# Kernel optimization log

Measured on AMD Instinct MI355X. Metric: run time of the kernel, lower is better.

## Reference

```python
import jax, jax.numpy as jnp
import numpy as np

GRID = 192          # grid_size (scaled up from the module's toy 32)
H = 0.1             # cell_size
VISC = 0.01         # viscosity
DT = 0.01           # config.time_step, passed as forward's dt
GRAV = 9.81


def setup_inputs() -> dict:
    key = jax.random.key(0)
    velocity_field = jax.random.normal(key, (3, GRID, GRID, GRID), dtype=jnp.float32)
    return {"velocity_field": velocity_field}


def _nb_sum(f):
    # 6-neighbor sum on the interior of the last three axes
    return (f[..., 2:, 1:-1, 1:-1] + f[..., :-2, 1:-1, 1:-1]
            + f[..., 1:-1, 2:, 1:-1] + f[..., 1:-1, :-2, 1:-1]
            + f[..., 1:-1, 1:-1, 2:] + f[..., 1:-1, 1:-1, :-2])


def _fluid_step(vel):
    N = GRID
    dt = DT
    # --- add_gravity ---
    vel = vel.at[2].add(-GRAV * dt)
    # --- advect: semi-Lagrangian backtrace + trilinear interpolation ---
    coords = jnp.arange(N, dtype=vel.dtype)
    X, Y, Z = jnp.meshgrid(coords, coords, coords, indexing='ij')
    pos = jnp.stack([X, Y, Z]) - vel * (dt / H)        # [3,N,N,N] backtraced positions
    pos = jnp.clip(pos, 0.0, float(N - 2))
    i0 = jnp.floor(pos).astype(jnp.int32)              # base corner, i1 = i0+1 <= N-1
    w1 = pos - i0.astype(vel.dtype)
    w0 = 1.0 - w1
    ix, iy, iz = i0[0], i0[1], i0[2]
    wx0, wy0, wz0 = w0[0], w0[1], w0[2]
    wx1, wy1, wz1 = w1[0], w1[1], w1[2]

    def g(di, dj, dk):
        return vel[:, ix + di, iy + dj, iz + dk]        # gather -> [3,N,N,N]

    vel = (g(0, 0, 0) * wx0 * wy0 * wz0 + g(0, 0, 1) * wx0 * wy0 * wz1
           + g(0, 1, 0) * wx0 * wy1 * wz0 + g(0, 1, 1) * wx0 * wy1 * wz1
           + g(1, 0, 0) * wx1 * wy0 * wz0 + g(1, 0, 1) * wx1 * wy0 * wz1
           + g(1, 1, 0) * wx1 * wy1 * wz0 + g(1, 1, 1) * wx1 * wy1 * wz1)
    # --- diffuse: 5 Jacobi sweeps on the interior ---
    alpha = VISC * dt / (H * H)
    inv = 1.0 / (1.0 + 6.0 * alpha)
    for _ in range(5):
        interior = (vel[:, 1:-1, 1:-1, 1:-1] + alpha * _nb_sum(vel)) * inv
        vel = vel.at[:, 1:-1, 1:-1, 1:-1].set(interior)
    # --- project: central-difference divergence, 20 Jacobi pressure sweeps, gradient subtract ---
    div = jnp.zeros((N, N, N), vel.dtype)
    div_int = ((vel[0, 2:, 1:-1, 1:-1] - vel[0, :-2, 1:-1, 1:-1])
               + (vel[1, 1:-1, 2:, 1:-1] - vel[1, 1:-1, :-2, 1:-1])
               + (vel[2, 1:-1, 1:-1, 2:] - vel[2, 1:-1, 1:-1, :-2])) / (2.0 * H)
    div = div.at[1:-1, 1:-1, 1:-1].set(div_int)
    p = jnp.zeros_like(div)
    for _ in range(20):
        p = p.at[1:-1, 1:-1, 1:-1].set((div[1:-1, 1:-1, 1:-1] + _nb_sum(p)) / 6.0)
    inv2h = 1.0 / (2.0 * H)
    vel = vel.at[0, 1:-1, 1:-1, 1:-1].add(-(p[2:, 1:-1, 1:-1] - p[:-2, 1:-1, 1:-1]) * inv2h)
    vel = vel.at[1, 1:-1, 1:-1, 1:-1].add(-(p[1:-1, 2:, 1:-1] - p[1:-1, :-2, 1:-1]) * inv2h)
    vel = vel.at[2, 1:-1, 1:-1, 1:-1].add(-(p[1:-1, 1:-1, 2:] - p[1:-1, 1:-1, :-2]) * inv2h)
    return vel


def reference(velocity_field):
    return _fluid_step(velocity_field)
```

## Files before the change

kernel.cpp:

```cpp
#include <hip/hip_runtime.h>
#include <hip/hip_fp16.h>


constexpr int   N      = 192;
constexpr int   N2     = N * N;
constexpr int   N3     = N * N * N;
constexpr float GDT    = 9.81f * 0.01f;
constexpr float SCL    = 0.01f / 0.1f;
constexpr float ALPHA  = 0.01f * 0.01f / (0.1f * 0.1f);
constexpr float INVDIF = 1.0f / (1.0f + 6.0f * ALPHA);
constexpr float INV2H  = 1.0f / (2.0f * 0.1f);
constexpr float SIXTH  = 1.0f / 6.0f;

constexpr int NT4 = (N3 / 4) / 256;
constexpr int SLAB = NT4 / 8;

__device__ __forceinline__ int swz(int b) {
    return (b & 7) * SLAB + (b >> 3);
}

__device__ __forceinline__ void decomp(int id, int& i, int& j, int& k0) {
    i = id / N2;
    const int r = id - i * N2;
    j = r / N;
    k0 = r - j * N;
}

union H4u { ushort4 u; __half h[4]; };
__device__ __forceinline__ float4 ldh4(const __half* p) {
    H4u t; t.u = *(const ushort4*)p;
    return make_float4(__half2float(t.h[0]), __half2float(t.h[1]),
                       __half2float(t.h[2]), __half2float(t.h[3]));
}
__device__ __forceinline__ void sth4(__half* p, float x, float y, float z, float w) {
    H4u t;
    t.h[0] = __float2half(x); t.h[1] = __float2half(y);
    t.h[2] = __float2half(z); t.h[3] = __float2half(w);
    *(ushort4*)p = t.u;
}
__device__ __forceinline__ float ldh(const __half* p) { return __half2float(*p); }

__global__ __launch_bounds__(192) void k_advect(const float* __restrict__ vin,
                                                float* __restrict__ vout) {
    __shared__ float s[27 * 192];

    const int k   = threadIdx.x;
    const int lin = blockIdx.y * 192 + blockIdx.x;
    const int x   = lin & 7;
    const int q   = lin >> 3;
    const int il  = q % 24;
    const int j   = q / 24;
    const int i   = x * 24 + il;
    const int id  = (i * N + j) * N + k;

    {
        const int rsub = threadIdx.x / 48;
        const int col  = (threadIdx.x - rsub * 48) * 4;
#pragma unroll
        for (int p = 0; p < 7; ++p) {
            const int r = p * 4 + rsub;
            if (r < 27) {
                const int c   = r / 9;
                const int rem = r - c * 9;
                const int di  = rem / 3;
                const int dj  = rem - di * 3;
                const int gi  = min(max(i + di - 1, 0), N - 1);
                const int gj  = min(max(j + dj - 1, 0), N - 1);
                *(float4*)&s[r * 192 + col] =
                    *(const float4*)&vin[c * N3 + gi * N2 + gj * N + col];
            }
        }
    }
    __syncthreads();

    const float vx = s[4 * 192 + k];
    const float vy = s[13 * 192 + k];
    const float vz = s[22 * 192 + k] - GDT;

    float px = (float)i - vx * SCL;
    float py = (float)j - vy * SCL;
    float pz = (float)k - vz * SCL;
    const float hi = (float)(N - 2);
    px = fminf(fmaxf(px, 0.0f), hi);
    py = fminf(fmaxf(py, 0.0f), hi);
    pz = fminf(fmaxf(pz, 0.0f), hi);

    const int ix = (int)px;
    const int iy = (int)py;
    const int iz = (int)pz;

    float g[3][8];
    const bool in = (ix >= i - 1) & (ix <= i) & (iy >= j - 1) & (iy <= j);
    if (in) {
        const int li = ix - i + 1;
        const int lj = iy - j + 1;
#pragma unroll
        for (int c = 0; c < 3; ++c) {
            const int r00 = ((c * 3 + li) * 3 + lj) * 192 + iz;
            const int r01 = r00 + 192;
            const int r10 = r00 + 3 * 192;
            const int r11 = r10 + 192;
            g[c][0] = s[r00];     g[c][1] = s[r00 + 1];
            g[c][2] = s[r01];     g[c][3] = s[r01 + 1];
            g[c][4] = s[r10];     g[c][5] = s[r10 + 1];
            g[c][6] = s[r11];     g[c][7] = s[r11 + 1];
        }
    } else {
        const int base = (ix * N + iy) * N + iz;
#pragma unroll
        for (int c = 0; c < 3; ++c) {
            const float* f = vin + c * N3 + base;
            g[c][0] = f[0];      g[c][1] = f[1];
            g[c][2] = f[N];      g[c][3] = f[N + 1];
            g[c][4] = f[N2];     g[c][5] = f[N2 + 1];
            g[c][6] = f[N2 + N]; g[c][7] = f[N2 + N + 1];
        }
    }

    const float wx1 = px - (float)ix, wy1 = py - (float)iy, wz1 = pz - (float)iz;
    const float wx0 = 1.0f - wx1,     wy0 = 1.0f - wy1,     wz0 = 1.0f - wz1;
    const float w000 = wx0 * wy0 * wz0;
    const float w001 = wx0 * wy0 * wz1;
    const float w010 = wx0 * wy1 * wz0;
    const float w011 = wx0 * wy1 * wz1;
    const float w100 = wx1 * wy0 * wz0;
    const float w101 = wx1 * wy0 * wz1;
    const float w110 = wx1 * wy1 * wz0;
    const float w111 = wx1 * wy1 * wz1;

#pragma unroll
    for (int c = 0; c < 3; ++c) {
        float r = g[c][0] * w000 + g[c][1] * w001
                + g[c][2] * w010 + g[c][3] * w011
                + g[c][4] * w100 + g[c][5] * w101
                + g[c][6] * w110 + g[c][7] * w111;
        if (c == 2) r -= GDT;
        vout[c * N3 + id] = r;
    }
}

__global__ __launch_bounds__(256) void k_diffuse4(const float* __restrict__ vin,
                                                  float* __restrict__ vout) {
    const int gtid = swz(blockIdx.x) * 256 + threadIdx.x;
    const int id   = gtid << 2;
    int i, j, k0; decomp(id, i, j, k0);
    const int b = blockIdx.y * N3 + id;

    const float4 c = *(const float4*)(vin + b);
    float4 out = c;
    if (i != 0 && i != N - 1 && j != 0 && j != N - 1) {
        const float4 ip = *(const float4*)(vin + b + N2);
        const float4 im = *(const float4*)(vin + b - N2);
        const float4 jp = *(const float4*)(vin + b + N);
        const float4 jm = *(const float4*)(vin + b - N);
        const float  km = (k0 > 0)     ? vin[b - 1] : 0.0f;
        const float  kp = (k0 < N - 4) ? vin[b + 4] : 0.0f;
        out.x = (c.x + ALPHA * (im.x + ip.x + jm.x + jp.x + km  + c.y)) * INVDIF;
        out.y = (c.y + ALPHA * (im.y + ip.y + jm.y + jp.y + c.x + c.z)) * INVDIF;
        out.z = (c.z + ALPHA * (im.z + ip.z + jm.z + jp.z + c.y + c.w)) * INVDIF;
        out.w = (c.w + ALPHA * (im.w + ip.w + jm.w + jp.w + c.z + kp )) * INVDIF;
        if (k0 == 0)     out.x = c.x;
        if (k0 == N - 4) out.w = c.w;
    }
    *(float4*)(vout + b) = out;
}

__global__ __launch_bounds__(256) void k_div4(const float* __restrict__ v,
                                              __half* __restrict__ dv) {
    const int gtid = swz(blockIdx.x) * 256 + threadIdx.x;
    const int id   = gtid << 2;
    int i, j, k0; decomp(id, i, j, k0);

    float ox = 0.f, oy = 0.f, oz = 0.f, ow = 0.f;
    if (i != 0 && i != N - 1 && j != 0 && j != N - 1) {
        const float4 xp = *(const float4*)(v + id + N2);
        const float4 xm = *(const float4*)(v + id - N2);
        const float4 yp = *(const float4*)(v + N3 + id + N);
        const float4 ym = *(const float4*)(v + N3 + id - N);
        const float4 z  = *(const float4*)(v + 2 * N3 + id);
        const float  zm = (k0 > 0)     ? v[2 * N3 + id - 1] : 0.0f;
        const float  zp = (k0 < N - 4) ? v[2 * N3 + id + 4] : 0.0f;
        ox = ((xp.x - xm.x) + (yp.x - ym.x) + (z.y - zm )) * INV2H;
        oy = ((xp.y - xm.y) + (yp.y - ym.y) + (z.z - z.x)) * INV2H;
        oz = ((xp.z - xm.z) + (yp.z - ym.z) + (z.w - z.y)) * INV2H;
        ow = ((xp.w - xm.w) + (yp.w - ym.w) + (zp  - z.z)) * INV2H;
        if (k0 == 0)     ox = 0.f;
        if (k0 == N - 4) ow = 0.f;
    }
    sth4(dv + id, ox, oy, oz, ow);
}

__global__ __launch_bounds__(256) void k_p2_4(const __half* __restrict__ dv,
                                              __half* __restrict__ p) {
    const int gtid = swz(blockIdx.x) * 256 + threadIdx.x;
    const int id   = gtid << 2;
    int i, j, k0; decomp(id, i, j, k0);

    float ox = 0.f, oy = 0.f, oz = 0.f, ow = 0.f;
    if (i != 0 && i != N - 1 && j != 0 && j != N - 1) {
        const float4 c  = ldh4(dv + id);
        const float4 ip = ldh4(dv + id + N2);
        const float4 im = ldh4(dv + id - N2);
        const float4 jp = ldh4(dv + id + N);
        const float4 jm = ldh4(dv + id - N);
        const float  km = (k0 > 0)     ? ldh(dv + id - 1) : 0.0f;
        const float  kp = (k0 < N - 4) ? ldh(dv + id + 4) : 0.0f;
        ox = (c.x + (im.x + ip.x + jm.x + jp.x + km  + c.y) * SIXTH) * SIXTH;
        oy = (c.y + (im.y + ip.y + jm.y + jp.y + c.x + c.z) * SIXTH) * SIXTH;
        oz = (c.z + (im.z + ip.z + jm.z + jp.z + c.y + c.w) * SIXTH) * SIXTH;
        ow = (c.w + (im.w + ip.w + jm.w + jp.w + c.z + kp ) * SIXTH) * SIXTH;
        if (k0 == 0)     ox = 0.f;
        if (k0 == N - 4) ow = 0.f;
    }
    sth4(p + id, ox, oy, oz, ow);
}

__global__ __launch_bounds__(256) void k_jacobi4(const __half* __restrict__ pin,
                                                 const __half* __restrict__ dv,
                                                 __half* __restrict__ pout) {
    const int gtid = swz(blockIdx.x) * 256 + threadIdx.x;
    const int id   = gtid << 2;
    int i, j, k0; decomp(id, i, j, k0);

    float ox = 0.f, oy = 0.f, oz = 0.f, ow = 0.f;
    if (i != 0 && i != N - 1 && j != 0 && j != N - 1) {
        const float4 c  = ldh4(pin + id);
        const float4 ip = ldh4(pin + id + N2);
        const float4 im = ldh4(pin + id - N2);
        const float4 jp = ldh4(pin + id + N);
        const float4 jm = ldh4(pin + id - N);
        const float4 d  = ldh4(dv + id);
        const float  km = (k0 > 0)     ? ldh(pin + id - 1) : 0.0f;
        const float  kp = (k0 < N - 4) ? ldh(pin + id + 4) : 0.0f;
        ox = (d.x + im.x + ip.x + jm.x + jp.x + km  + c.y) * SIXTH;
        oy = (d.y + im.y + ip.y + jm.y + jp.y + c.x + c.z) * SIXTH;
        oz = (d.z + im.z + ip.z + jm.z + jp.z + c.y + c.w) * SIXTH;
        ow = (d.w + im.w + ip.w + jm.w + jp.w + c.z + kp ) * SIXTH;
        if (k0 == 0)     ox = 0.f;
        if (k0 == N - 4) ow = 0.f;
    }
    sth4(pout + id, ox, oy, oz, ow);
}

__global__ __launch_bounds__(256) void k_grad4(float* __restrict__ vel,
                                               const __half* __restrict__ p) {
    const int gtid = swz(blockIdx.x) * 256 + threadIdx.x;
    const int id   = gtid << 2;
    int i, j, k0; decomp(id, i, j, k0);
    if (i == 0 || i == N - 1 || j == 0 || j == N - 1) return;

    const float4 xp = ldh4(p + id + N2);
    const float4 xm = ldh4(p + id - N2);
    const float4 yp = ldh4(p + id + N);
    const float4 ym = ldh4(p + id - N);
    const float4 c  = ldh4(p + id);
    const float  pm = (k0 > 0)     ? ldh(p + id - 1) : 0.0f;
    const float  pp = (k0 < N - 4) ? ldh(p + id + 4) : 0.0f;

    const bool bx = (k0 == 0);
    const bool bw = (k0 == N - 4);

    float4 v0 = *(float4*)(vel + id);
    if (!bx) v0.x -= (xp.x - xm.x) * INV2H;
             v0.y -= (xp.y - xm.y) * INV2H;
             v0.z -= (xp.z - xm.z) * INV2H;
    if (!bw) v0.w -= (xp.w - xm.w) * INV2H;
    *(float4*)(vel + id) = v0;

    float4 v1 = *(float4*)(vel + N3 + id);
    if (!bx) v1.x -= (yp.x - ym.x) * INV2H;
             v1.y -= (yp.y - ym.y) * INV2H;
             v1.z -= (yp.z - ym.z) * INV2H;
    if (!bw) v1.w -= (yp.w - ym.w) * INV2H;
    *(float4*)(vel + N3 + id) = v1;

    float4 v2 = *(float4*)(vel + 2 * N3 + id);
    if (!bx) v2.x -= (c.y - pm ) * INV2H;
             v2.y -= (c.z - c.x) * INV2H;
             v2.z -= (c.w - c.y) * INV2H;
    if (!bw) v2.w -= (pp  - c.z) * INV2H;
    *(float4*)(vel + 2 * N3 + id) = v2;
}

extern "C" void kernel_launch(void* const* d_in, const int* in_sizes, int n_in,
                              void* d_out, int out_size, void* d_ws, size_t ws_size,
                              hipStream_t stream) {
    const float* vin  = (const float*)d_in[0];
    float*       vout = (float*)d_out;
    float*       ws   = (float*)d_ws;

    float*  velB = ws;
    __half* hws  = (__half*)d_ws;
    __half* dv   = hws;
    __half* pA   = hws + N3;
    __half* pB   = hws + 2 * N3;

    const dim3 blk(N, 1, 1);
    const dim3 grid1(N, N, 1);
    const dim3 blk4(256, 1, 1);
    const dim3 grid4_1(NT4, 1, 1);
    const dim3 grid4_3(NT4, 3, 1);

    k_advect<<<grid1, blk, 0, stream>>>(vin, velB);

    k_diffuse4<<<grid4_3, blk4, 0, stream>>>(velB, vout);
    k_diffuse4<<<grid4_3, blk4, 0, stream>>>(vout, velB);
    k_diffuse4<<<grid4_3, blk4, 0, stream>>>(velB, vout);
    k_diffuse4<<<grid4_3, blk4, 0, stream>>>(vout, velB);
    k_diffuse4<<<grid4_3, blk4, 0, stream>>>(velB, vout);

    k_div4<<<grid4_1, blk4, 0, stream>>>(vout, dv);
    k_p2_4<<<grid4_1, blk4, 0, stream>>>(dv, pA);
    __half* pin  = pA;
    __half* pout = pB;
    for (int s = 0; s < 18; ++s) {
        k_jacobi4<<<grid4_1, blk4, 0, stream>>>(pin, dv, pout);
        __half* t = pin; pin = pout; pout = t;
    }
    k_grad4<<<grid4_1, blk4, 0, stream>>>(vout, pin);
}
```

Measured before the change: 576.0 us.

## Tile advection over 2x2 (i,j) pencils per block to share staged halo

```diff
diff --git a/kernel.cpp b/kernel.cpp
--- a/kernel.cpp
+++ b/kernel.cpp
@@ -40,42 +40,51 @@
 }
 __device__ __forceinline__ float ldh(const __half* p) { return __half2float(*p); }
 
-__global__ __launch_bounds__(192) void k_advect(const float* __restrict__ vin,
+constexpr int RS    = 196;
+constexpr int TILEI = N / 2;
+constexpr int TPS   = TILEI / 8;
+constexpr int NBADV = (N / 2) * (N / 2);
+
+__global__ __launch_bounds__(768) void k_advect(const float* __restrict__ vin,
                                                 float* __restrict__ vout) {
-    __shared__ float s[27 * 192];
-
-    const int k   = threadIdx.x;
-    const int lin = blockIdx.y * 192 + blockIdx.x;
+    __shared__ float s[48 * RS];
+
+    const int lin = blockIdx.x;
     const int x   = lin & 7;
     const int q   = lin >> 3;
-    const int il  = q % 24;
-    const int j   = q / 24;
-    const int i   = x * 24 + il;
-    const int id  = (i * N + j) * N + k;
-
-    {
-        const int rsub = threadIdx.x / 48;
-        const int col  = (threadIdx.x - rsub * 48) * 4;
+    const int il  = q % TPS;
+    const int jt  = q / TPS;
+    const int i0  = (x * TPS + il) * 2;
+    const int j0  = jt * 2;
+
 #pragma unroll
-        for (int p = 0; p < 7; ++p) {
-            const int r = p * 4 + rsub;
-            if (r < 27) {
-                const int c   = r / 9;
-                const int rem = r - c * 9;
-                const int di  = rem / 3;
-                const int dj  = rem - di * 3;
-                const int gi  = min(max(i + di - 1, 0), N - 1);
-                const int gj  = min(max(j + dj - 1, 0), N - 1);
-                *(float4*)&s[r * 192 + col] =
-                    *(const float4*)&vin[c * N3 + gi * N2 + gj * N + col];
-            }
-        }
+    for (int p = 0; p < 3; ++p) {
+        const int f   = p * 768 + threadIdx.x;
+        const int r   = f / 48;
+        const int c4  = f - r * 48;
+        const int c   = r >> 4;
+        const int rem = r & 15;
+        const int di  = rem >> 2;
+        const int dj  = rem & 3;
+        const int gi  = min(max(i0 + di - 1, 0), N - 1);
+        const int gj  = min(max(j0 + dj - 1, 0), N - 1);
+        *(float4*)&s[r * RS + c4 * 4] =
+            *(const float4*)&vin[c * N3 + gi * N2 + gj * N + c4 * 4];
     }
     __syncthreads();
 
-    const float vx = s[4 * 192 + k];
-    const float vy = s[13 * 192 + k];
-    const float vz = s[22 * 192 + k] - GDT;
+    const int t  = threadIdx.x / 192;
+    const int k  = threadIdx.x - t * 192;
+    const int li = t >> 1;
+    const int lj = t & 1;
+    const int i  = i0 + li;
+    const int j  = j0 + lj;
+    const int id = (i * N + j) * N + k;
+
+    const int cr = ((li + 1) * 4 + (lj + 1)) * RS + k;
+    const float vx = s[cr];
+    const float vy = s[16 * RS + cr];
+    const float vz = s[32 * RS + cr] - GDT;
 
     float px = (float)i - vx * SCL;
     float py = (float)j - vy * SCL;
@@ -92,14 +101,14 @@
     float g[3][8];
     const bool in = (ix >= i - 1) & (ix <= i) & (iy >= j - 1) & (iy <= j);
     if (in) {
-        const int li = ix - i + 1;
-        const int lj = iy - j + 1;
+        const int lix = ix - i0 + 1;
+        const int liy = iy - j0 + 1;
 #pragma unroll
         for (int c = 0; c < 3; ++c) {
-            const int r00 = ((c * 3 + li) * 3 + lj) * 192 + iz;
-            const int r01 = r00 + 192;
-            const int r10 = r00 + 3 * 192;
-            const int r11 = r10 + 192;
+            const int r00 = ((c * 16 + lix * 4 + liy)) * RS + iz;
+            const int r01 = r00 + RS;
+            const int r10 = r00 + 4 * RS;
+            const int r11 = r10 + RS;
             g[c][0] = s[r00];     g[c][1] = s[r00 + 1];
             g[c][2] = s[r01];     g[c][3] = s[r01 + 1];
             g[c][4] = s[r10];     g[c][5] = s[r10 + 1];
@@ -295,13 +304,13 @@
     __half* pA   = hws + N3;
     __half* pB   = hws + 2 * N3;
 
-    const dim3 blk(N, 1, 1);
-    const dim3 grid1(N, N, 1);
+    const dim3 blkA(768, 1, 1);
+    const dim3 gridA(NBADV, 1, 1);
     const dim3 blk4(256, 1, 1);
     const dim3 grid4_1(NT4, 1, 1);
     const dim3 grid4_3(NT4, 3, 1);
 
-    k_advect<<<grid1, blk, 0, stream>>>(vin, velB);
+    k_advect<<<gridA, blkA, 0, stream>>>(vin, velB);
 
     k_diffuse4<<<grid4_3, blk4, 0, stream>>>(velB, vout);
     k_diffuse4<<<grid4_3, blk4, 0, stream>>>(vout, velB);
```

After: 531.5 us. 1.08x faster.
